# Kernel optimization log

Hardware: AMD Instinct MI355X
Metric: run time of the kernel (lower is better)

Reference implementation:

```python
import jax, jax.numpy as jnp
import numpy as np

N = 20000   # nodes
E = 320000  # edges (avg degree 16)
H = 4       # heads
C = 128     # per-head / output channels (concat=False -> mean over heads)
IN = 2      # init_channels (TSP coords)
NEG_SLOPE = 0.2


def setup_inputs() -> dict:
    key = jax.random.key(0)
    ks = jax.random.split(key, 32)
    s = 0.1
    def W(k, shape):
        return (jax.random.normal(k, shape, jnp.float32) * s)
    inp = {
        "x": jax.random.normal(ks[0], (N, IN), jnp.float32),
        "edge_index": jax.random.randint(ks[1], (2, E), 0, N, jnp.int32),
        "edge_attr": jax.random.uniform(ks[2], (E, 1), jnp.float32),
    }
    i = 3
    for b in range(2):  # two parallel GATBlocks
        inp[f"Wsrc{b}"]  = W(ks[i+0], (IN, H * C))
        inp[f"bsrc{b}"]  = jnp.zeros((H * C,), jnp.float32)
        inp[f"Wdst{b}"]  = W(ks[i+1], (IN, H * C))
        inp[f"bdst{b}"]  = jnp.zeros((H * C,), jnp.float32)
        inp[f"Wedge{b}"] = W(ks[i+2], (1, H * C))
        inp[f"att{b}"]   = W(ks[i+3], (H, C))
        inp[f"bias{b}"]  = jnp.zeros((C,), jnp.float32)
        inp[f"Wres{b}"]  = W(ks[i+4], (IN, C))  # SkipConnection projection (2 -> 128)
        i += 5
    inp["Wfuse"] = W(ks[i], (2 * C, C))
    inp["bfuse"] = jnp.zeros((C,), jnp.float32)
    return inp


def _gat_block(x, src, dst, ea, Wsrc, bsrc, Wdst, bdst, Wedge, att, bias, Wres):
    # GATv2Conv (concat=False) + ReLU + residual projection
    xs = (x @ Wsrc + bsrc).reshape(N, H, C)   # lin_l (source / message)
    xd = (x @ Wdst + bdst).reshape(N, H, C)   # lin_r (target)
    ee = (ea @ Wedge).reshape(-1, H, C)       # lin_edge
    e = jax.nn.leaky_relu(xs[src] + xd[dst] + ee, NEG_SLOPE)  # [Etot,H,C]
    logits = jnp.einsum('ehc,hc->eh', e, att)                 # [Etot,H]
    # segment softmax over incoming edges of each target node
    m = jax.ops.segment_max(logits, dst, num_segments=N)
    m = jnp.where(jnp.isfinite(m), m, 0.0)
    p = jnp.exp(logits - m[dst])
    denom = jax.ops.segment_sum(p, dst, num_segments=N)
    alpha = p / (denom[dst] + 1e-16)                          # [Etot,H]
    agg = jax.ops.segment_sum(xs[src] * alpha[:, :, None], dst, num_segments=N)
    out = agg.mean(axis=1) + bias                             # concat=False: mean heads
    return jax.nn.relu(out) + x @ Wres                        # ReLU then skip add


def reference(x, edge_index, edge_attr,
              Wsrc0, bsrc0, Wdst0, bdst0, Wedge0, att0, bias0, Wres0,
              Wsrc1, bsrc1, Wdst1, bdst1, Wedge1, att1, bias1, Wres1,
              Wfuse, bfuse):
    src, dst = edge_index[0], edge_index[1]
    # PyG default add_self_loops=True, fill_value='mean' for edge_attr
    loop = jnp.arange(N, dtype=src.dtype)
    src_a = jnp.concatenate([src, loop])
    dst_a = jnp.concatenate([dst, loop])
    mean_attr = jnp.mean(edge_attr, axis=0, keepdims=True)
    ea = jnp.concatenate([edge_attr, jnp.broadcast_to(mean_attr, (N, 1))], axis=0)

    h0 = _gat_block(x, src_a, dst_a, ea, Wsrc0, bsrc0, Wdst0, bdst0, Wedge0, att0, bias0, Wres0)
    h1 = _gat_block(x, src_a, dst_a, ea, Wsrc1, bsrc1, Wdst1, bdst1, Wedge1, att1, bias1, Wres1)
    xc = jnp.concatenate([h0, h1], axis=-1)       # [N, 2C]
    return jax.nn.relu(xc @ Wfuse + bfuse)        # [N, C]
```

## Files before the change

kernel.cpp:

```cpp
#include <hip/hip_runtime.h>

#define HH 4
#define CC 128
#define NPB 64

typedef __attribute__((ext_vector_type(8))) short short8v;
typedef __attribute__((ext_vector_type(4))) float f32x4;

static inline size_t roundup256(size_t x) { return (x + 255) & ~(size_t)255; }

static __device__ __forceinline__ unsigned short f2bf(float f) {
    unsigned int u = __float_as_uint(f);
    unsigned int r = (u + 0x7FFFu + ((u >> 16) & 1u)) >> 16;
    return (unsigned short)r;
}

__global__ __launch_bounds__(256) void prep_kernel(
    const int* __restrict__ ei, const float* __restrict__ eattr,
    float* __restrict__ meansum, float* __restrict__ Lin, int* __restrict__ cnt,
    const float* __restrict__ Wsrc0, const float* __restrict__ bsrc0,
    const float* __restrict__ Wdst0, const float* __restrict__ bdst0,
    const float* __restrict__ Wedge0, const float* __restrict__ att0,
    const float* __restrict__ Wsrc1, const float* __restrict__ bsrc1,
    const float* __restrict__ Wdst1, const float* __restrict__ bdst1,
    const float* __restrict__ Wedge1, const float* __restrict__ att1,
    const float* __restrict__ Wfuse,
    float* __restrict__ packed, unsigned short* __restrict__ pwB, int E)
{
    int tid = blockIdx.x * 256 + threadIdx.x;
    int lane = threadIdx.x & 63, wid = threadIdx.x >> 6;
    float s = 0.f;
    if (tid < E) {
        atomicAdd(&cnt[ei[E + tid]], 1);
        s = eattr[tid];
    }
    #pragma unroll
    for (int off = 32; off > 0; off >>= 1) s += __shfl_down(s, off, 64);
    __shared__ float wsum[4];
    if (lane == 0) wsum[wid] = s;
    __syncthreads();
    if (threadIdx.x == 0)
        atomicAdd(meansum, wsum[0] + wsum[1] + wsum[2] + wsum[3]);

    if (blockIdx.x < 4) {
        int b = tid >> 9;
        int hc = tid & 511;
        int c = hc & 127;
        int h = hc >> 7;
        int bh = b * 4 + h;
        const float* Ws = b ? Wsrc1 : Wsrc0;
        const float* bs = b ? bsrc1 : bsrc0;
        const float* Wd = b ? Wdst1 : Wdst0;
        const float* bd = b ? bdst1 : bdst0;
        const float* We = b ? Wedge1 : Wedge0;
        const float* at = b ? att1 : att0;
        float A = Ws[hc], B = Ws[512 + hc];
        float C = Wd[hc], D = Wd[512 + hc];
        float Ec = We[hc];
        float F = bs[hc] + bd[hc];
        float a = at[hc];
        float4* r = (float4*)(packed + ((size_t)(bh * 128 + c)) * 8);
        r[0] = make_float4(A, B, C, D);
        r[1] = make_float4(Ec, F, 0.4f * a, 0.f);
        float sa = 0.6f * a;
        float vals[6] = {sa * A, sa * B, sa * C, sa * D, sa * Ec, sa * F};
        #pragma unroll
        for (int k = 0; k < 6; ++k) {
            float v = vals[k];
            #pragma unroll
            for (int off = 32; off > 0; off >>= 1) v += __shfl_down(v, off, 64);
            vals[k] = v;
        }
        __shared__ float Ls[4][6];
        if (lane == 0) {
            #pragma unroll
            for (int k = 0; k < 6; ++k) Ls[wid][k] = vals[k];
        }
        __syncthreads();
        if (threadIdx.x < 12) {
            int w2 = threadIdx.x / 6;
            int k = threadIdx.x % 6;
            int bhg = blockIdx.x * 2 + w2;
            Lin[bhg * 6 + k] = Ls[w2 * 2][k] + Ls[w2 * 2 + 1][k];
        }
    }

    if (blockIdx.x >= 4 && blockIdx.x < 20) {
        int t2 = tid - 1024;
        int ct = t2 >> 9;
        int kc = (t2 >> 6) & 7;
        int l  = t2 & 63;
        int c = ct * 16 + (l & 15);
        int kb = kc * 32 + (l >> 4) * 8;
        unsigned short v[8];
        #pragma unroll
        for (int j = 0; j < 8; ++j)
            v[j] = f2bf(Wfuse[(kb + j) * CC + c]);
        unsigned short* dst = pwB + (size_t)t2 * 8;
        #pragma unroll
        for (int j = 0; j < 8; ++j) dst[j] = v[j];
    }
}

__global__ __launch_bounds__(1024) void scan_kernel(const int* __restrict__ cnt,
                                                    int* __restrict__ rowptr,
                                                    int* __restrict__ cur, int N) {
    const int CH = 32;
    int t = threadIdx.x;
    int base = t * CH;
    int local[CH];
    int s = 0;
    #pragma unroll
    for (int i = 0; i < CH; ++i) {
        int idx = base + i;
        int v = (idx < N) ? cnt[idx] + 1 : 0;
        local[i] = s;
        s += v;
    }
    __shared__ int sums[1024];
    sums[t] = s;
    __syncthreads();
    for (int off = 1; off < 1024; off <<= 1) {
        int v = (t >= off) ? sums[t - off] : 0;
        __syncthreads();
        sums[t] += v;
        __syncthreads();
    }
    int excl = sums[t] - s;
    #pragma unroll
    for (int i = 0; i < CH; ++i) {
        int idx = base + i;
        if (idx < N) {
            int v = excl + local[i];
            rowptr[idx] = v;
            cur[idx] = v;
        }
    }
    if (t == 1023) rowptr[N] = excl + s;
}

__global__ __launch_bounds__(256) void scatter_kernel(
    const int* __restrict__ ei, const float* __restrict__ x,
    const float* __restrict__ eattr, const float* __restrict__ meansum,
    int* __restrict__ cur, float4* __restrict__ ed4, float* __restrict__ ea1,
    int* __restrict__ esrc, int N, int E) {
    int e = blockIdx.x * 256 + threadIdx.x;
    int Etot = E + N;
    if (e >= Etot) return;
    int src, dst;
    float ea;
    if (e < E) { src = ei[e]; dst = ei[E + e]; ea = eattr[e]; }
    else       { src = e - E; dst = src; ea = meansum[0] / (float)E; }
    int pos = atomicAdd(&cur[dst], 1);
    const float2* x2 = (const float2*)x;
    float2 xs = x2[src];
    float2 xd = x2[dst];
    ed4[pos] = make_float4(xs.x, xs.y, xd.x, xd.y);
    ea1[pos] = ea;
    esrc[pos] = src;
}

__global__ __launch_bounds__(256) void logits_kernel(
    const float4* __restrict__ ed4,
    const float* __restrict__ ea1,
    const float* __restrict__ Lin,
    const float4* __restrict__ pw,
    float* __restrict__ p8, int EtotPad, int nchunks)
{
    int blk = blockIdx.x;
    int bh = blk / nchunks;
    int chunk = blk - bh * nchunks;
    int t = threadIdx.x;
    int iA = chunk * 512 + t;
    int iB = iA + 256;
    float4 eA = ed4[iA], eB = ed4[iB];
    float aA = ea1[iA], aB = ea1[iB];

    const float4* wp = pw + (size_t)bh * 256;
    float a0 = 0.f, a1 = 0.f;
    #pragma unroll 8
    for (int c = 0; c < 128; ++c) {
        float4 w0 = wp[2 * c];
        float4 w1 = wp[2 * c + 1];
        float uA = fmaf(w0.x, eA.x,
                   fmaf(w0.y, eA.y,
                   fmaf(w0.z, eA.z,
                   fmaf(w0.w, eA.w,
                   fmaf(w1.x, aA, w1.y)))));
        float uB = fmaf(w0.x, eB.x,
                   fmaf(w0.y, eB.y,
                   fmaf(w0.z, eB.z,
                   fmaf(w0.w, eB.w,
                   fmaf(w1.x, aB, w1.y)))));
        a0 = fmaf(w1.z, __builtin_fabsf(uA), a0);
        a1 = fmaf(w1.z, __builtin_fabsf(uB), a1);
    }

    const float* Lp = Lin + bh * 6;
    float lgA = fmaf(Lp[0], eA.x, fmaf(Lp[1], eA.y, fmaf(Lp[2], eA.z,
                fmaf(Lp[3], eA.w, fmaf(Lp[4], aA, Lp[5]))))) + a0;
    float lgB = fmaf(Lp[0], eB.x, fmaf(Lp[1], eB.y, fmaf(Lp[2], eB.z,
                fmaf(Lp[3], eB.w, fmaf(Lp[4], aB, Lp[5]))))) + a1;
    float* plane = p8 + (size_t)bh * EtotPad;
    plane[iA] = __expf(lgA);
    plane[iB] = __expf(lgB);
}

__global__ __launch_bounds__(512) void node_kernel(
    const float* __restrict__ x,
    const int* __restrict__ rowptr,
    const int* __restrict__ esrc,
    const float* __restrict__ p8,
    const float* __restrict__ Wsrc0, const float* __restrict__ bsrc0,
    const float* __restrict__ bias0, const float* __restrict__ Wres0,
    const float* __restrict__ Wsrc1, const float* __restrict__ bsrc1,
    const float* __restrict__ bias1, const float* __restrict__ Wres1,
    const unsigned short* __restrict__ pwB, const float* __restrict__ bfuse,
    float* __restrict__ out, int N, int EtotPad)
{
    __shared__ __align__(16) unsigned short hb[NPB][264];
    __shared__ __align__(16) float Sl[NPB][24];
    int t = threadIdx.x;
    int n0 = blockIdx.x * NPB;
    const float2* x2 = (const float2*)x;

    {
        int g = t >> 3, bh = t & 7;
        int n = n0 + g;
        if (n < N) {
            int beg = rowptr[n], end = rowptr[n + 1];
            const float* plane = p8 + (size_t)bh * EtotPad;
            float s0 = 0.f, s1 = 0.f, sb = 0.f;
            for (int i = beg; i < end; ++i) {
                float p = plane[i];
                int srcu = esrc[i];
                float2 xs = x2[srcu];
                s0 = fmaf(p, xs.x, s0);
                s1 = fmaf(p, xs.y, s1);
                sb += p;
            }
            float rin = 1.f / (sb + 1e-16f);
            Sl[g][bh * 3 + 0] = s0 * rin;
            Sl[g][bh * 3 + 1] = s1 * rin;
            Sl[g][bh * 3 + 2] = sb * rin;
        }
    }
    __syncthreads();

    int c = t & (CC - 1);
    int quarter = t >> 7;

    float w00[HH], w01[HH], wb0[HH], w10[HH], w11[HH], wb1[HH];
    #pragma unroll
    for (int h = 0; h < HH; ++h) {
        w00[h] = Wsrc0[h * CC + c];
        w01[h] = Wsrc0[512 + h * CC + c];
        wb0[h] = bsrc0[h * CC + c];
        w10[h] = Wsrc1[h * CC + c];
        w11[h] = Wsrc1[512 + h * CC + c];
        wb1[h] = bsrc1[h * CC + c];
    }
    float bi0 = bias0[c], bi1 = bias1[c];
    float r00 = Wres0[c], r01 = Wres0[CC + c];
    float r10 = Wres1[c], r11 = Wres1[CC + c];

    for (int ni = quarter; ni < NPB; ni += 4) {
        int n = n0 + ni;
        if (n < N) {
            float x0 = x[2 * n], x1 = x[2 * n + 1];
            const float4* Sp4 = (const float4*)&Sl[ni][0];
            float4 q0 = Sp4[0], q1 = Sp4[1], q2 = Sp4[2];
            float4 q3 = Sp4[3], q4 = Sp4[4], q5 = Sp4[5];
            float h0v, h1v;
            {
                float s0[HH] = {q0.x, q0.w, q1.z, q2.y};
                float s1[HH] = {q0.y, q1.x, q1.w, q2.z};
                float sb[HH] = {q0.z, q1.y, q2.x, q2.w};
                float acc = 0.f;
                #pragma unroll
                for (int h = 0; h < HH; ++h)
                    acc += fmaf(w00[h], s0[h], fmaf(w01[h], s1[h], wb0[h] * sb[h]));
                float o = fmaxf(acc * 0.25f + bi0, 0.f);
                h0v = o + x0 * r00 + x1 * r01;
            }
            {
                float s0[HH] = {q3.x, q3.w, q4.z, q5.y};
                float s1[HH] = {q3.y, q4.x, q4.w, q5.z};
                float sb[HH] = {q3.z, q4.y, q5.x, q5.w};
                float acc = 0.f;
                #pragma unroll
                for (int h = 0; h < HH; ++h)
                    acc += fmaf(w10[h], s0[h], fmaf(w11[h], s1[h], wb1[h] * sb[h]));
                float o = fmaxf(acc * 0.25f + bi1, 0.f);
                h1v = o + x0 * r10 + x1 * r11;
            }
            hb[ni][c] = f2bf(h0v);
            hb[ni][CC + c] = f2bf(h1v);
        }
    }
    __syncthreads();

    int w = t >> 6;
    int l = t & 63;
    int nt = w & 3;
    int cthalf = w >> 2;
    int row = nt * 16 + (l & 15);

    short8v a[8];
    #pragma unroll
    for (int kc = 0; kc < 8; ++kc)
        a[kc] = *reinterpret_cast<const short8v*>(&hb[row][kc * 32 + (l >> 4) * 8]);

    const short8v* pB = reinterpret_cast<const short8v*>(pwB);
    #pragma unroll
    for (int ci = 0; ci < 4; ++ci) {
        int ct = cthalf * 4 + ci;
        f32x4 acc = {0.f, 0.f, 0.f, 0.f};
        #pragma unroll
        for (int kc = 0; kc < 8; ++kc) {
            short8v b = pB[(ct * 8 + kc) * 64 + l];
            acc = __builtin_amdgcn_mfma_f32_16x16x32_bf16(a[kc], b, acc, 0, 0, 0);
        }
        int ch = ct * 16 + (l & 15);
        float bi = bfuse[ch];
        #pragma unroll
        for (int j = 0; j < 4; ++j) {
            int n = n0 + nt * 16 + (l >> 4) * 4 + j;
            if (n < N) out[(size_t)n * CC + ch] = fmaxf(acc[j] + bi, 0.f);
        }
    }
}

extern "C" void kernel_launch(void* const* d_in, const int* in_sizes, int n_in,
                              void* d_out, int out_size, void* d_ws, size_t ws_size,
                              hipStream_t stream) {
    const float* x      = (const float*)d_in[0];
    const int*   ei     = (const int*)d_in[1];
    const float* eattr  = (const float*)d_in[2];
    const float* Wsrc0  = (const float*)d_in[3];
    const float* bsrc0  = (const float*)d_in[4];
    const float* Wdst0  = (const float*)d_in[5];
    const float* bdst0  = (const float*)d_in[6];
    const float* Wedge0 = (const float*)d_in[7];
    const float* att0   = (const float*)d_in[8];
    const float* bias0  = (const float*)d_in[9];
    const float* Wres0  = (const float*)d_in[10];
    const float* Wsrc1  = (const float*)d_in[11];
    const float* bsrc1  = (const float*)d_in[12];
    const float* Wdst1  = (const float*)d_in[13];
    const float* bdst1  = (const float*)d_in[14];
    const float* Wedge1 = (const float*)d_in[15];
    const float* att1   = (const float*)d_in[16];
    const float* bias1  = (const float*)d_in[17];
    const float* Wres1  = (const float*)d_in[18];
    const float* Wfuse  = (const float*)d_in[19];
    const float* bfuse  = (const float*)d_in[20];
    float* out = (float*)d_out;

    int N = in_sizes[0] / 2;
    int E = in_sizes[1] / 2;
    int Etot = E + N;
    int EtotPad = (Etot + 511) & ~511;

    size_t off = 0;
    float* meansum = (float*)((char*)d_ws + off);  off += 256;
    int*   cnt     = (int*)((char*)d_ws + off);    off += roundup256((size_t)N * sizeof(int));
    size_t zero_bytes = off;
    float* Lin     = (float*)((char*)d_ws + off);  off += 256;
    int*   cur     = (int*)((char*)d_ws + off);    off += roundup256((size_t)N * sizeof(int));
    int*   rowptr  = (int*)((char*)d_ws + off);    off += roundup256((size_t)(N + 1) * sizeof(int));
    float* packed  = (float*)((char*)d_ws + off);  off += roundup256(8 * 128 * 8 * sizeof(float));
    unsigned short* pwB = (unsigned short*)((char*)d_ws + off);
                                                   off += roundup256(4096 * 8 * sizeof(unsigned short));
    float4* ed4    = (float4*)((char*)d_ws + off); off += roundup256((size_t)EtotPad * sizeof(float4));
    float* ea1     = (float*)((char*)d_ws + off);  off += roundup256((size_t)EtotPad * sizeof(float));
    int*   esrc    = (int*)((char*)d_ws + off);    off += roundup256((size_t)EtotPad * sizeof(int));
    float* p8      = (float*)((char*)d_ws + off);  off += roundup256((size_t)EtotPad * 8 * sizeof(float));

    hipMemsetAsync(d_ws, 0, zero_bytes, stream);

    prep_kernel<<<(E + 255) / 256, 256, 0, stream>>>(
        ei, eattr, meansum, Lin, cnt,
        Wsrc0, bsrc0, Wdst0, bdst0, Wedge0, att0,
        Wsrc1, bsrc1, Wdst1, bdst1, Wedge1, att1,
        Wfuse, packed, pwB, E);

    scan_kernel<<<1, 1024, 0, stream>>>(cnt, rowptr, cur, N);

    scatter_kernel<<<(Etot + 255) / 256, 256, 0, stream>>>(
        ei, x, eattr, meansum, cur, ed4, ea1, esrc, N, E);

    int nchunks = EtotPad / 512;
    logits_kernel<<<8 * nchunks, 256, 0, stream>>>(
        ed4, ea1, Lin, (const float4*)packed, p8, EtotPad, nchunks);

    node_kernel<<<(N + NPB - 1) / NPB, 512, 0, stream>>>(
        x, rowptr, esrc, p8,
        Wsrc0, bsrc0, bias0, Wres0,
        Wsrc1, bsrc1, bias1, Wres1,
        pwB, bfuse, out, N, EtotPad);
}
```

Baseline: 162.6 us.

## Use wave-shuffle scan, process two heads per logits block, split node edge loop

The single-block scan now does a wavefront shuffle scan with a small cross-wave pass, replacing the shared-memory Hillis-Steele loop and its many barriers. The logits kernel handles two block-head pairs per block, so each edge record is loaded once for both and half as many blocks are launched. The node kernel's softmax aggregation splits each node's edge list across two lanes and combines them with a shuffle, which shortens the serial per-thread gather loop. The costs are longer per-thread work in logits, fewer blocks to fill the GPU, and two passes over nodes in the aggregation phase.

```diff
diff --git a/kernel.cpp b/kernel.cpp
--- a/kernel.cpp
+++ b/kernel.cpp
@@ -107,26 +107,35 @@
                                                     int* __restrict__ cur, int N) {
     const int CH = 32;
     int t = threadIdx.x;
+    int lane = t & 63, wid = t >> 6;
     int base = t * CH;
     int local[CH];
-    int s = 0;
+    int own = 0;
     #pragma unroll
     for (int i = 0; i < CH; ++i) {
         int idx = base + i;
         int v = (idx < N) ? cnt[idx] + 1 : 0;
-        local[i] = s;
-        s += v;
-    }
-    __shared__ int sums[1024];
-    sums[t] = s;
+        local[i] = own;
+        own += v;
+    }
+    int incl = own;
+    #pragma unroll
+    for (int off = 1; off < 64; off <<= 1) {
+        int v = __shfl_up(incl, off, 64);
+        if (lane >= off) incl += v;
+    }
+    __shared__ int wtot[16];
+    __shared__ int wexcl[17];
+    if (lane == 63) wtot[wid] = incl;
     __syncthreads();
-    for (int off = 1; off < 1024; off <<= 1) {
-        int v = (t >= off) ? sums[t - off] : 0;
-        __syncthreads();
-        sums[t] += v;
-        __syncthreads();
-    }
-    int excl = sums[t] - s;
+    if (t == 0) {
+        int acc = 0;
+        #pragma unroll
+        for (int w = 0; w < 16; ++w) { wexcl[w] = acc; acc += wtot[w]; }
+        wexcl[16] = acc;
+    }
+    __syncthreads();
+    int excl = wexcl[wid] + (incl - own);
     #pragma unroll
     for (int i = 0; i < CH; ++i) {
         int idx = base + i;
@@ -136,7 +145,7 @@
             cur[idx] = v;
         }
     }
-    if (t == 1023) rowptr[N] = excl + s;
+    if (t == 1023) rowptr[N] = wexcl[16];
 }
 
 __global__ __launch_bounds__(256) void scatter_kernel(
@@ -168,42 +177,45 @@
     float* __restrict__ p8, int EtotPad, int nchunks)
 {
     int blk = blockIdx.x;
-    int bh = blk / nchunks;
-    int chunk = blk - bh * nchunks;
+    int bhp = blk / nchunks;
+    int chunk = blk - bhp * nchunks;
     int t = threadIdx.x;
     int iA = chunk * 512 + t;
     int iB = iA + 256;
     float4 eA = ed4[iA], eB = ed4[iB];
     float aA = ea1[iA], aB = ea1[iB];
 
-    const float4* wp = pw + (size_t)bh * 256;
-    float a0 = 0.f, a1 = 0.f;
-    #pragma unroll 8
-    for (int c = 0; c < 128; ++c) {
-        float4 w0 = wp[2 * c];
-        float4 w1 = wp[2 * c + 1];
-        float uA = fmaf(w0.x, eA.x,
-                   fmaf(w0.y, eA.y,
-                   fmaf(w0.z, eA.z,
-                   fmaf(w0.w, eA.w,
-                   fmaf(w1.x, aA, w1.y)))));
-        float uB = fmaf(w0.x, eB.x,
-                   fmaf(w0.y, eB.y,
-                   fmaf(w0.z, eB.z,
-                   fmaf(w0.w, eB.w,
-                   fmaf(w1.x, aB, w1.y)))));
-        a0 = fmaf(w1.z, __builtin_fabsf(uA), a0);
-        a1 = fmaf(w1.z, __builtin_fabsf(uB), a1);
-    }
-
-    const float* Lp = Lin + bh * 6;
-    float lgA = fmaf(Lp[0], eA.x, fmaf(Lp[1], eA.y, fmaf(Lp[2], eA.z,
-                fmaf(Lp[3], eA.w, fmaf(Lp[4], aA, Lp[5]))))) + a0;
-    float lgB = fmaf(Lp[0], eB.x, fmaf(Lp[1], eB.y, fmaf(Lp[2], eB.z,
-                fmaf(Lp[3], eB.w, fmaf(Lp[4], aB, Lp[5]))))) + a1;
-    float* plane = p8 + (size_t)bh * EtotPad;
-    plane[iA] = __expf(lgA);
-    plane[iB] = __expf(lgB);
+    #pragma unroll
+    for (int bi = 0; bi < 2; ++bi) {
+        int bh = bhp * 2 + bi;
+        const float4* wp = pw + (size_t)bh * 256;
+        float a0 = 0.f, a1 = 0.f;
+        #pragma unroll 8
+        for (int c = 0; c < 128; ++c) {
+            float4 w0 = wp[2 * c];
+            float4 w1 = wp[2 * c + 1];
+            float uA = fmaf(w0.x, eA.x,
+                       fmaf(w0.y, eA.y,
+                       fmaf(w0.z, eA.z,
+                       fmaf(w0.w, eA.w,
+                       fmaf(w1.x, aA, w1.y)))));
+            float uB = fmaf(w0.x, eB.x,
+                       fmaf(w0.y, eB.y,
+                       fmaf(w0.z, eB.z,
+                       fmaf(w0.w, eB.w,
+                       fmaf(w1.x, aB, w1.y)))));
+            a0 = fmaf(w1.z, __builtin_fabsf(uA), a0);
+            a1 = fmaf(w1.z, __builtin_fabsf(uB), a1);
+        }
+        const float* Lp = Lin + bh * 6;
+        float lgA = fmaf(Lp[0], eA.x, fmaf(Lp[1], eA.y, fmaf(Lp[2], eA.z,
+                    fmaf(Lp[3], eA.w, fmaf(Lp[4], aA, Lp[5]))))) + a0;
+        float lgB = fmaf(Lp[0], eB.x, fmaf(Lp[1], eB.y, fmaf(Lp[2], eB.z,
+                    fmaf(Lp[3], eB.w, fmaf(Lp[4], aB, Lp[5]))))) + a1;
+        float* plane = p8 + (size_t)bh * EtotPad;
+        plane[iA] = __expf(lgA);
+        plane[iB] = __expf(lgB);
+    }
 }
 
 __global__ __launch_bounds__(512) void node_kernel(
@@ -225,24 +237,36 @@
     const float2* x2 = (const float2*)x;
 
     {
-        int g = t >> 3, bh = t & 7;
-        int n = n0 + g;
-        if (n < N) {
-            int beg = rowptr[n], end = rowptr[n + 1];
-            const float* plane = p8 + (size_t)bh * EtotPad;
-            float s0 = 0.f, s1 = 0.f, sb = 0.f;
-            for (int i = beg; i < end; ++i) {
-                float p = plane[i];
-                int srcu = esrc[i];
-                float2 xs = x2[srcu];
-                s0 = fmaf(p, xs.x, s0);
-                s1 = fmaf(p, xs.y, s1);
-                sb += p;
+        int g = t >> 4;
+        int sub = t & 15;
+        int bh = sub & 7;
+        int half = sub >> 3;
+        const float* plane = p8 + (size_t)bh * EtotPad;
+        #pragma unroll
+        for (int pass = 0; pass < 2; ++pass) {
+            int ni = g + pass * 32;
+            int n = n0 + ni;
+            if (n < N) {
+                int beg = rowptr[n], end = rowptr[n + 1];
+                float s0 = 0.f, s1 = 0.f, sb = 0.f;
+                for (int i = beg + half; i < end; i += 2) {
+                    float p = plane[i];
+                    int srcu = esrc[i];
+                    float2 xs = x2[srcu];
+                    s0 = fmaf(p, xs.x, s0);
+                    s1 = fmaf(p, xs.y, s1);
+                    sb += p;
+                }
+                s0 += __shfl_xor(s0, 8, 64);
+                s1 += __shfl_xor(s1, 8, 64);
+                sb += __shfl_xor(sb, 8, 64);
+                if (half == 0) {
+                    float rin = 1.f / (sb + 1e-16f);
+                    Sl[ni][bh * 3 + 0] = s0 * rin;
+                    Sl[ni][bh * 3 + 1] = s1 * rin;
+                    Sl[ni][bh * 3 + 2] = sb * rin;
+                }
             }
-            float rin = 1.f / (sb + 1e-16f);
-            Sl[g][bh * 3 + 0] = s0 * rin;
-            Sl[g][bh * 3 + 1] = s1 * rin;
-            Sl[g][bh * 3 + 2] = sb * rin;
         }
     }
     __syncthreads();
@@ -391,7 +415,7 @@
         ei, x, eattr, meansum, cur, ed4, ea1, esrc, N, E);
 
     int nchunks = EtotPad / 512;
-    logits_kernel<<<8 * nchunks, 256, 0, stream>>>(
+    logits_kernel<<<4 * nchunks, 256, 0, stream>>>(
         ed4, ea1, Lin, (const float4*)packed, p8, EtotPad, nchunks);
 
     node_kernel<<<(N + NPB - 1) / NPB, 512, 0, stream>>>(
```

New measurement: 166.3 us. 1.02x slower.
